# Performance work log

Measured on AMD Instinct MI355X. Metric: run time of the kernel, lower is better.

The kernel has to match this reference:

```python
import jax, jax.numpy as jnp
import numpy as np

SIGMA = 1.0


def _rbf_gram(A, B):
    # A: (Tb, N, C), B: (Tb, M, C) -> (Tb, N, M)
    AA = jnp.sum(A * A, axis=2, keepdims=True)          # (Tb, N, 1)
    BB = jnp.sum(B * B, axis=2, keepdims=True)          # (Tb, M, 1)
    d = AA + jnp.swapaxes(BB, 1, 2) - 2.0 * jnp.einsum('bnc,bmc->bnm', A, B)
    return jnp.exp(-d / (2.0 * SIGMA ** 2))


def setup_inputs() -> dict:
    key = jax.random.key(0)
    kx, ky = jax.random.split(key)
    x = jax.random.normal(kx, (512, 128, 16), dtype=jnp.float32)
    y = jax.random.normal(ky, (512, 128, 16), dtype=jnp.float32)
    return {"x": x, "y": y}


def reference(x, y):
    # x, y: (batch, stream, channel)
    x_fds = jnp.concatenate((x[:, :-1, :], x[:, 1:, :]), axis=1)  # (B, 2(T-1), C)
    y_fds = jnp.concatenate((y[:, :-1, :], y[:, 1:, :]), axis=1)
    xf = jnp.transpose(x_fds, (1, 0, 2))  # (2(T-1), B, C)
    yf = jnp.transpose(y_fds, (1, 0, 2))

    N = xf.shape[1]
    Kxx = _rbf_gram(xf, xf)  # (2(T-1), N, N)
    # off-diagonal mean per batch: (sum - trace) / (N*(N-1))
    e_xx = (Kxx.sum(axis=(1, 2)) - jnp.trace(Kxx, axis1=1, axis2=2)) / (N * (N - 1))
    E_k_x1_x2 = e_xx.mean()

    Kxy = _rbf_gram(xf, yf)
    E_k_x_y = Kxy.mean(axis=(1, 2)).mean()

    return E_k_x1_x2 - 2.0 * E_k_x_y
```

## Files before the change

kernel.cpp:

```cpp
#include <hip/hip_runtime.h>


#define LOG2E 1.4426950408889634f
#define SCALE 1.2011224087864498f

#define XH_OFF   0u
#define XL_OFF   524288u
#define YH_OFF   1048576u
#define YL_OFF   1572864u
#define GX_OFF   2097152u
#define CSX_OFF  2162688u
#define CSY_OFF  2228224u
#define PART_OFF 2293760u

typedef __attribute__((ext_vector_type(8))) __bf16 bf16x8;
typedef __attribute__((ext_vector_type(4))) float floatx4;

union FragU { uint4 q; unsigned int u[4]; bf16x8 v; };

static __device__ __forceinline__ int off(int n) { return (n << 3) + ((n >> 2) << 2); }

static __device__ __forceinline__ unsigned short bfbits(__bf16 h) {
    union { __bf16 h; unsigned short s; } u; u.h = h; return u.s;
}
static __device__ __forceinline__ unsigned int packhh(__bf16 a, __bf16 b) {
    return (unsigned int)bfbits(a) | ((unsigned int)bfbits(b) << 16);
}

__global__ __launch_bounds__(256) void prep_kernel(const float* __restrict__ x,
                                                   const float* __restrict__ y,
                                                   unsigned int* __restrict__ ws) {
    const int bid = blockIdx.x, tid = threadIdx.x;
    const int m   = bid >> 8;
    const int t   = (bid >> 1) & 127;
    const int row = ((bid & 1) << 8) + tid;

    const float4* __restrict__ src4 = m ? (const float4*)y : (const float4*)x;
    const size_t gb = (size_t)row * 512 + t * 4;
    float4 f0 = src4[gb], f1 = src4[gb + 1], f2 = src4[gb + 2], f3 = src4[gb + 3];
    const float fs[16] = { f0.x, f0.y, f0.z, f0.w, f1.x, f1.y, f1.z, f1.w,
                           f2.x, f2.y, f2.z, f2.w, f3.x, f3.y, f3.z, f3.w };
    float g = 0.f;
    unsigned int hw[8], lw[8];
#pragma unroll
    for (int p = 0; p < 8; ++p) {
        const float v0 = fs[2 * p], v1 = fs[2 * p + 1];
        g += v0 * v0 + v1 * v1;
        const float s0 = v0 * SCALE, s1 = v1 * SCALE;
        const __bf16 h0 = (__bf16)s0, h1 = (__bf16)s1;
        hw[p] = packhh(h0, h1);
        lw[p] = packhh((__bf16)(s0 - (float)h0), (__bf16)(s1 - (float)h1));
    }
    const float gp = 0.5f * LOG2E * g;
    const unsigned int idx = (unsigned int)t * 512u + (unsigned int)row;
    unsigned int* __restrict__ H = ws + (m ? YH_OFF : XH_OFF) + (size_t)idx * 8;
    unsigned int* __restrict__ L = ws + (m ? YL_OFF : XL_OFF) + (size_t)idx * 8;
    *(uint4*)&H[0] = make_uint4(hw[0], hw[1], hw[2], hw[3]);
    *(uint4*)&H[4] = make_uint4(hw[4], hw[5], hw[6], hw[7]);
    *(uint4*)&L[0] = make_uint4(lw[0], lw[1], lw[2], lw[3]);
    *(uint4*)&L[4] = make_uint4(lw[4], lw[5], lw[6], lw[7]);
    float* __restrict__ wsf = (float*)ws;
    wsf[(m ? CSY_OFF : CSX_OFF) + idx] = __builtin_amdgcn_exp2f(-gp);
    if (!m) wsf[GX_OFF + idx] = gp;
}

__global__ __launch_bounds__(256, 4) void gram_kernel(const unsigned int* __restrict__ ws,
                                                      float* __restrict__ part) {
    __shared__ unsigned int XHs[1152], XLs[1152], YHs[1152], YLs[1152];
    __shared__ float csx[128], csy[128];
    __shared__ float srg[256];
    __shared__ float red[8];

    const int bid   = blockIdx.x;
    const int t     = bid >> 3;
    const int strip = (bid >> 2) & 1;
    const int jq    = bid & 3;
    const int tid   = threadIdx.x;
    const int w     = tid >> 6;
    const int lane  = tid & 63;
    const int quad  = lane >> 4;
    const int l15   = lane & 15;
    const int qh    = quad & 1;
    const float* __restrict__ wsf = (const float*)ws;

    {
        const int a = tid >> 6, idx = tid & 63;
        const unsigned int abase = (a == 0) ? XH_OFF : (a == 1) ? XL_OFF
                                 : (a == 2) ? YH_OFF : YL_OFF;
        const unsigned int* __restrict__ gsrc =
            ws + abase + ((size_t)t * 512 + jq * 128) * 8 + (size_t)idx * 16;
        uint4 q0 = *(const uint4*)&gsrc[0];
        uint4 q1 = *(const uint4*)&gsrc[4];
        uint4 q2 = *(const uint4*)&gsrc[8];
        uint4 q3 = *(const uint4*)&gsrc[12];
        unsigned int* __restrict__ dst = (a == 0) ? XHs : (a == 1) ? XLs
                                       : (a == 2) ? YHs : YLs;
        const int r0 = idx * 2;
        *(uint4*)&dst[off(r0)]         = q0;
        *(uint4*)&dst[off(r0) + 4]     = q1;
        *(uint4*)&dst[off(r0 + 1)]     = q2;
        *(uint4*)&dst[off(r0 + 1) + 4] = q3;
    }
    if (tid < 128) csx[tid]       = wsf[CSX_OFF + t * 512 + jq * 128 + tid];
    else           csy[tid - 128] = wsf[CSY_OFF + t * 512 + jq * 128 + (tid - 128)];
    srg[tid] = wsf[GX_OFF + t * 512 + strip * 256 + tid];

    bf16x8 a1f[4], a2f[4];
    {
        FragU z; z.q = make_uint4(0u, 0u, 0u, 0u);
        const unsigned int hbase = (quad < 2) ? XH_OFF : XL_OFF;
#pragma unroll
        for (int rt = 0; rt < 4; ++rt) {
            const int row = strip * 256 + w * 64 + rt * 16 + l15;
            const unsigned int* __restrict__ p =
                ws + hbase + ((size_t)t * 512 + row) * 8 + qh * 4;
            FragU u; u.q = *(const uint4*)p;
            a1f[rt] = u.v;
            a2f[rt] = (quad < 2) ? u.v : z.v;
        }
    }
    __syncthreads();

    float sxx[4][4], sxy[4][4];
#pragma unroll
    for (int rt = 0; rt < 4; ++rt)
#pragma unroll
        for (int r = 0; r < 4; ++r) { sxx[rt][r] = 0.f; sxy[rt][r] = 0.f; }

    for (int jt = 0; jt < 8; ++jt) {
        const int n  = jt * 16 + l15;
        const int rb = off(n) + qh * 4;
        FragU bh, bl, ch, cl;
        bh.q = *(const uint4*)&XHs[rb];
        bl.q = *(const uint4*)&XLs[rb];
        ch.q = *(const uint4*)&YHs[rb];
        cl.q = *(const uint4*)&YLs[rb];
        const float cx = csx[n];
        const float cy = csy[n];
#pragma unroll
        for (int rt = 0; rt < 4; ++rt) {
            floatx4 c = {0.f, 0.f, 0.f, 0.f};
            c = __builtin_amdgcn_mfma_f32_16x16x32_bf16(a1f[rt], bh.v, c, 0, 0, 0);
            c = __builtin_amdgcn_mfma_f32_16x16x32_bf16(a2f[rt], bl.v, c, 0, 0, 0);
#pragma unroll
            for (int r = 0; r < 4; ++r)
                sxx[rt][r] = fmaf(__builtin_amdgcn_exp2f(c[r]), cx, sxx[rt][r]);
            floatx4 d = {0.f, 0.f, 0.f, 0.f};
            d = __builtin_amdgcn_mfma_f32_16x16x32_bf16(a1f[rt], ch.v, d, 0, 0, 0);
            d = __builtin_amdgcn_mfma_f32_16x16x32_bf16(a2f[rt], cl.v, d, 0, 0, 0);
#pragma unroll
            for (int r = 0; r < 4; ++r)
                sxy[rt][r] = fmaf(__builtin_amdgcn_exp2f(d[r]), cy, sxy[rt][r]);
        }
    }

    float txx = 0.f, txy = 0.f;
#pragma unroll
    for (int rt = 0; rt < 4; ++rt)
#pragma unroll
        for (int r = 0; r < 4; ++r) {
            const float rs = __builtin_amdgcn_exp2f(-srg[w * 64 + rt * 16 + quad * 4 + r]);
            txx = fmaf(sxx[rt][r], rs, txx);
            txy = fmaf(sxy[rt][r], rs, txy);
        }
    for (int o = 32; o > 0; o >>= 1) {
        txx += __shfl_down(txx, o, 64);
        txy += __shfl_down(txy, o, 64);
    }
    if (lane == 0) { red[w] = txx; red[4 + w] = txy; }
    __syncthreads();
    if (tid == 0) {
        const float wt = (t == 0 || t == 127) ? 1.f : 2.f;
        part[bid]        = wt * (red[0] + red[1] + red[2] + red[3]);
        part[1024 + bid] = wt * (red[4] + red[5] + red[6] + red[7]);
    }
}

__global__ __launch_bounds__(256) void finalize_kernel(const float* __restrict__ part,
                                                       float* __restrict__ out) {
    const int tid = threadIdx.x;
    double vxx = 0.0, vxy = 0.0;
#pragma unroll
    for (int k = 0; k < 4; ++k) {
        vxx += (double)part[tid + 256 * k];
        vxy += (double)part[1024 + tid + 256 * k];
    }
    for (int o = 32; o > 0; o >>= 1) {
        vxx += __shfl_down(vxx, o, 64);
        vxy += __shfl_down(vxy, o, 64);
    }
    __shared__ double red[8];
    const int wid = tid >> 6;
    if ((tid & 63) == 0) { red[wid] = vxx; red[4 + wid] = vxy; }
    __syncthreads();
    if (tid == 0) {
        double sxx = red[0] + red[1] + red[2] + red[3];
        double sxy = red[4] + red[5] + red[6] + red[7];
        double e1 = (sxx - 254.0 * 512.0) / (254.0 * 512.0 * 511.0);
        double e2 = sxy / (254.0 * 512.0 * 512.0);
        out[0] = (float)(e1 - 2.0 * e2);
    }
}

extern "C" void kernel_launch(void* const* d_in, const int* in_sizes, int n_in,
                              void* d_out, int out_size, void* d_ws, size_t ws_size,
                              hipStream_t stream) {
    (void)in_sizes; (void)n_in; (void)out_size; (void)ws_size;
    const float* x = (const float*)d_in[0];
    const float* y = (const float*)d_in[1];
    float* out = (float*)d_out;
    unsigned int* ws = (unsigned int*)d_ws;
    float* part = (float*)d_ws + PART_OFF;

    prep_kernel<<<dim3(512), dim3(256), 0, stream>>>(x, y, ws);
    gram_kernel<<<dim3(1024), dim3(256), 0, stream>>>(ws, part);
    finalize_kernel<<<dim3(1), dim3(256), 0, stream>>>(part, out);
}
```

Before: 79.63 us.

## Exploit Kxx symmetry with triangular block tiling and software-pipeline MFMA/exp

Result: no change. 79.68 us (+0.1%).

```diff
diff --git a/kernel.cpp b/kernel.cpp
--- a/kernel.cpp
+++ b/kernel.cpp
@@ -66,54 +66,55 @@
 
 __global__ __launch_bounds__(256, 4) void gram_kernel(const unsigned int* __restrict__ ws,
                                                       float* __restrict__ part) {
-    __shared__ unsigned int XHs[1152], XLs[1152], YHs[1152], YLs[1152];
-    __shared__ float csx[128], csy[128];
-    __shared__ float srg[256];
-    __shared__ float red[8];
-
-    const int bid   = blockIdx.x;
-    const int t     = bid >> 3;
-    const int strip = (bid >> 2) & 1;
-    const int jq    = bid & 3;
-    const int tid   = threadIdx.x;
-    const int w     = tid >> 6;
-    const int lane  = tid & 63;
-    const int quad  = lane >> 4;
-    const int l15   = lane & 15;
-    const int qh    = quad & 1;
+    __shared__ unsigned int BH[1152], BL[1152];
+    __shared__ float csB[128], srg[128];
+    __shared__ float red[4];
+
+    const int slot = blockIdx.x;
+    const int t    = blockIdx.y;
+    const int tid  = threadIdx.x;
+    const int w    = tid >> 6;
+    const int lane = tid & 63;
+    const int quad = lane >> 4;
+    const int l15  = lane & 15;
+    const int qh   = quad & 1;
     const float* __restrict__ wsf = (const float*)ws;
 
+    int sa, sq, isxx;
+    if (slot < 16) { isxx = 0; sa = slot >> 2; sq = slot & 3; }
+    else {
+        isxx = 1;
+        const int s = slot - 16;
+        if      (s < 4) { sa = 0; sq = s; }
+        else if (s < 7) { sa = 1; sq = s - 3; }
+        else if (s < 9) { sa = 2; sq = s - 5; }
+        else            { sa = 3; sq = 3; }
+    }
+
     {
-        const int a = tid >> 6, idx = tid & 63;
-        const unsigned int abase = (a == 0) ? XH_OFF : (a == 1) ? XL_OFF
-                                 : (a == 2) ? YH_OFF : YL_OFF;
-        const unsigned int* __restrict__ gsrc =
-            ws + abase + ((size_t)t * 512 + jq * 128) * 8 + (size_t)idx * 16;
-        uint4 q0 = *(const uint4*)&gsrc[0];
-        uint4 q1 = *(const uint4*)&gsrc[4];
-        uint4 q2 = *(const uint4*)&gsrc[8];
-        uint4 q3 = *(const uint4*)&gsrc[12];
-        unsigned int* __restrict__ dst = (a == 0) ? XHs : (a == 1) ? XLs
-                                       : (a == 2) ? YHs : YLs;
-        const int r0 = idx * 2;
-        *(uint4*)&dst[off(r0)]         = q0;
-        *(uint4*)&dst[off(r0) + 4]     = q1;
-        *(uint4*)&dst[off(r0 + 1)]     = q2;
-        *(uint4*)&dst[off(r0 + 1) + 4] = q3;
-    }
-    if (tid < 128) csx[tid]       = wsf[CSX_OFF + t * 512 + jq * 128 + tid];
-    else           csy[tid - 128] = wsf[CSY_OFF + t * 512 + jq * 128 + (tid - 128)];
-    srg[tid] = wsf[GX_OFF + t * 512 + strip * 256 + tid];
-
-    bf16x8 a1f[4], a2f[4];
+        const int r = tid & 127;
+        const unsigned int base = isxx ? ((tid < 128) ? XH_OFF : XL_OFF)
+                                       : ((tid < 128) ? YH_OFF : YL_OFF);
+        const unsigned int* __restrict__ g =
+            ws + base + (unsigned int)((t * 512 + sq * 128 + r) << 3);
+        uint4 q0 = *(const uint4*)&g[0];
+        uint4 q1 = *(const uint4*)&g[4];
+        unsigned int* __restrict__ dst = (tid < 128) ? BH : BL;
+        *(uint4*)&dst[off(r)]     = q0;
+        *(uint4*)&dst[off(r) + 4] = q1;
+        if (tid < 128) csB[r] = wsf[(isxx ? CSX_OFF : CSY_OFF) + t * 512 + sq * 128 + r];
+        else           srg[r] = wsf[GX_OFF + t * 512 + sa * 128 + r];
+    }
+
+    bf16x8 a1f[2], a2f[2];
     {
         FragU z; z.q = make_uint4(0u, 0u, 0u, 0u);
         const unsigned int hbase = (quad < 2) ? XH_OFF : XL_OFF;
 #pragma unroll
-        for (int rt = 0; rt < 4; ++rt) {
-            const int row = strip * 256 + w * 64 + rt * 16 + l15;
+        for (int rt = 0; rt < 2; ++rt) {
+            const int row = sa * 128 + w * 32 + rt * 16 + l15;
             const unsigned int* __restrict__ p =
-                ws + hbase + ((size_t)t * 512 + row) * 8 + qh * 4;
+                ws + hbase + (unsigned int)((t * 512 + row) << 3) + qh * 4;
             FragU u; u.q = *(const uint4*)p;
             a1f[rt] = u.v;
             a2f[rt] = (quad < 2) ? u.v : z.v;
@@ -121,70 +122,77 @@
     }
     __syncthreads();
 
-    float sxx[4][4], sxy[4][4];
-#pragma unroll
-    for (int rt = 0; rt < 4; ++rt)
-#pragma unroll
-        for (int r = 0; r < 4; ++r) { sxx[rt][r] = 0.f; sxy[rt][r] = 0.f; }
-
-    for (int jt = 0; jt < 8; ++jt) {
+    float sum[2][4] = {{0.f, 0.f, 0.f, 0.f}, {0.f, 0.f, 0.f, 0.f}};
+
+    floatx4 accP[2], accC[2];
+    float csP;
+    {
+        const int rb = off(l15) + qh * 4;
+        FragU bh, bl;
+        bh.q = *(const uint4*)&BH[rb];
+        bl.q = *(const uint4*)&BL[rb];
+        csP = csB[l15];
+        floatx4 zc = {0.f, 0.f, 0.f, 0.f};
+        accP[0] = __builtin_amdgcn_mfma_f32_16x16x32_bf16(a1f[0], bh.v, zc, 0, 0, 0);
+        accP[0] = __builtin_amdgcn_mfma_f32_16x16x32_bf16(a2f[0], bl.v, accP[0], 0, 0, 0);
+        accP[1] = __builtin_amdgcn_mfma_f32_16x16x32_bf16(a1f[1], bh.v, zc, 0, 0, 0);
+        accP[1] = __builtin_amdgcn_mfma_f32_16x16x32_bf16(a2f[1], bl.v, accP[1], 0, 0, 0);
+    }
+#pragma unroll
+    for (int jt = 1; jt < 8; ++jt) {
         const int n  = jt * 16 + l15;
         const int rb = off(n) + qh * 4;
-        FragU bh, bl, ch, cl;
-        bh.q = *(const uint4*)&XHs[rb];
-        bl.q = *(const uint4*)&XLs[rb];
-        ch.q = *(const uint4*)&YHs[rb];
-        cl.q = *(const uint4*)&YLs[rb];
-        const float cx = csx[n];
-        const float cy = csy[n];
-#pragma unroll
-        for (int rt = 0; rt < 4; ++rt) {
-            floatx4 c = {0.f, 0.f, 0.f, 0.f};
-            c = __builtin_amdgcn_mfma_f32_16x16x32_bf16(a1f[rt], bh.v, c, 0, 0, 0);
-            c = __builtin_amdgcn_mfma_f32_16x16x32_bf16(a2f[rt], bl.v, c, 0, 0, 0);
+        FragU bh, bl;
+        bh.q = *(const uint4*)&BH[rb];
+        bl.q = *(const uint4*)&BL[rb];
+        const float cs = csB[n];
+        floatx4 zc = {0.f, 0.f, 0.f, 0.f};
+        accC[0] = __builtin_amdgcn_mfma_f32_16x16x32_bf16(a1f[0], bh.v, zc, 0, 0, 0);
+        accC[0] = __builtin_amdgcn_mfma_f32_16x16x32_bf16(a2f[0], bl.v, accC[0], 0, 0, 0);
+        accC[1] = __builtin_amdgcn_mfma_f32_16x16x32_bf16(a1f[1], bh.v, zc, 0, 0, 0);
+        accC[1] = __builtin_amdgcn_mfma_f32_16x16x32_bf16(a2f[1], bl.v, accC[1], 0, 0, 0);
+#pragma unroll
+        for (int rt = 0; rt < 2; ++rt)
 #pragma unroll
             for (int r = 0; r < 4; ++r)
-                sxx[rt][r] = fmaf(__builtin_amdgcn_exp2f(c[r]), cx, sxx[rt][r]);
-            floatx4 d = {0.f, 0.f, 0.f, 0.f};
-            d = __builtin_amdgcn_mfma_f32_16x16x32_bf16(a1f[rt], ch.v, d, 0, 0, 0);
-            d = __builtin_amdgcn_mfma_f32_16x16x32_bf16(a2f[rt], cl.v, d, 0, 0, 0);
-#pragma unroll
-            for (int r = 0; r < 4; ++r)
-                sxy[rt][r] = fmaf(__builtin_amdgcn_exp2f(d[r]), cy, sxy[rt][r]);
+                sum[rt][r] = fmaf(__builtin_amdgcn_exp2f(accP[rt][r]), csP, sum[rt][r]);
+        accP[0] = accC[0];
+        accP[1] = accC[1];
+        csP = cs;
+    }
+#pragma unroll
+    for (int rt = 0; rt < 2; ++rt)
+#pragma unroll
+        for (int r = 0; r < 4; ++r)
+            sum[rt][r] = fmaf(__builtin_amdgcn_exp2f(accP[rt][r]), csP, sum[rt][r]);
+
+    float tot = 0.f;
+#pragma unroll
+    for (int rt = 0; rt < 2; ++rt)
+#pragma unroll
+        for (int r = 0; r < 4; ++r) {
+            const float rs = __builtin_amdgcn_exp2f(-srg[w * 32 + rt * 16 + quad * 4 + r]);
+            tot = fmaf(sum[rt][r], rs, tot);
         }
-    }
-
-    float txx = 0.f, txy = 0.f;
-#pragma unroll
-    for (int rt = 0; rt < 4; ++rt)
-#pragma unroll
-        for (int r = 0; r < 4; ++r) {
-            const float rs = __builtin_amdgcn_exp2f(-srg[w * 64 + rt * 16 + quad * 4 + r]);
-            txx = fmaf(sxx[rt][r], rs, txx);
-            txy = fmaf(sxy[rt][r], rs, txy);
-        }
-    for (int o = 32; o > 0; o >>= 1) {
-        txx += __shfl_down(txx, o, 64);
-        txy += __shfl_down(txy, o, 64);
-    }
-    if (lane == 0) { red[w] = txx; red[4 + w] = txy; }
+    for (int o = 32; o > 0; o >>= 1) tot += __shfl_down(tot, o, 64);
+    if (lane == 0) red[w] = tot;
     __syncthreads();
     if (tid == 0) {
-        const float wt = (t == 0 || t == 127) ? 1.f : 2.f;
-        part[bid]        = wt * (red[0] + red[1] + red[2] + red[3]);
-        part[1024 + bid] = wt * (red[4] + red[5] + red[6] + red[7]);
+        float wt = (t == 0 || t == 127) ? 1.f : 2.f;
+        if (isxx && sq > sa) wt *= 2.f;
+        const int idx = isxx ? (2048 + t * 10 + (slot - 16)) : (t * 16 + slot);
+        part[idx] = wt * (red[0] + red[1] + red[2] + red[3]);
     }
 }
 
 __global__ __launch_bounds__(256) void finalize_kernel(const float* __restrict__ part,
                                                        float* __restrict__ out) {
     const int tid = threadIdx.x;
-    double vxx = 0.0, vxy = 0.0;
-#pragma unroll
-    for (int k = 0; k < 4; ++k) {
-        vxx += (double)part[tid + 256 * k];
-        vxy += (double)part[1024 + tid + 256 * k];
-    }
+    double vxy = 0.0, vxx = 0.0;
+#pragma unroll
+    for (int k = 0; k < 8; ++k)  vxy += (double)part[tid + 256 * k];
+#pragma unroll
+    for (int k = 8; k < 13; ++k) vxx += (double)part[tid + 256 * k];
     for (int o = 32; o > 0; o >>= 1) {
         vxx += __shfl_down(vxx, o, 64);
         vxy += __shfl_down(vxy, o, 64);
@@ -213,6 +221,6 @@
     float* part = (float*)d_ws + PART_OFF;
 
     prep_kernel<<<dim3(512), dim3(256), 0, stream>>>(x, y, ws);
-    gram_kernel<<<dim3(1024), dim3(256), 0, stream>>>(ws, part);
+    gram_kernel<<<dim3(26, 128), dim3(256), 0, stream>>>(ws, part);
     finalize_kernel<<<dim3(1), dim3(256), 0, stream>>>(part, out);
 }
```
